# Kernel optimization log

Measured on AMD Instinct MI355X. Metric: run time of the kernel, lower is better.

Reference implementation:

```python
import jax, jax.numpy as jnp
import numpy as np

N_GRAPHS = 32   # number of graphs (equal-size contiguous segments in `batch`)
SEG_LEN = 512   # nodes per graph
NUM_HEADS = 16
LN_EPS = 1e-5


def setup_inputs() -> dict:
    key = jax.random.key(0)
    ks = jax.random.split(key, 4)
    N = N_GRAPHS * SEG_LEN
    D = 1024
    x = jax.random.normal(ks[0], (N, D), dtype=jnp.float32)
    # contiguous equal-size graph segments (what per-graph batching produces)
    batch = jnp.repeat(jnp.arange(N_GRAPHS, dtype=jnp.int64), SEG_LEN)
    s = 1.0 / np.sqrt(D)
    w_in = jax.random.normal(ks[1], (3 * D, D), dtype=jnp.float32) * s
    b_in = jnp.zeros((3 * D,), dtype=jnp.float32)
    w_out = jax.random.normal(ks[2], (D, D), dtype=jnp.float32) * s
    b_out = jnp.zeros((D,), dtype=jnp.float32)
    gamma = jnp.ones((D,), dtype=jnp.float32)
    beta = jnp.zeros((D,), dtype=jnp.float32)
    return {"x": x, "batch": batch, "w_in": w_in, "b_in": b_in,
            "w_out": w_out, "b_out": b_out, "gamma": gamma, "beta": beta}


def _mha_blockdiag(x, w_in, b_in, w_out, b_out):
    # Packed per-graph self-attention: identical math to looping MHA over each
    # graph's node subset, but done in one dense batched attention.
    N, D = x.shape
    G, S, H = N_GRAPHS, SEG_LEN, NUM_HEADS
    dh = D // H
    qkv = x @ w_in.T + b_in                       # (N, 3D)
    qkv = qkv.reshape(G, S, 3, H, dh)
    q, k, v = qkv[:, :, 0], qkv[:, :, 1], qkv[:, :, 2]  # (G, S, H, dh)
    scale = 1.0 / jnp.sqrt(jnp.asarray(dh, x.dtype))
    scores = jnp.einsum('gqhd,gkhd->ghqk', q, k) * scale  # (G, H, S, S)
    probs = jax.nn.softmax(scores, axis=-1)
    ctx = jnp.einsum('ghqk,gkhd->gqhd', probs, v).reshape(N, D)
    return ctx @ w_out.T + b_out


def reference(x, batch, w_in, b_in, w_out, b_out, gamma, beta):
    attn_out = _mha_blockdiag(x, w_in, b_in, w_out, b_out)
    # dropout is identity in eval mode; residual + LayerNorm
    h = x + attn_out
    mu = jnp.mean(h, axis=-1, keepdims=True)
    var = jnp.var(h, axis=-1, keepdims=True)
    return (h - mu) * jax.lax.rsqrt(var + LN_EPS) * gamma + beta
```

## Files before the change

kernel.cpp:

```cpp
#include <hip/hip_runtime.h>
#include <hip/hip_bf16.h>
#include <math.h>

#define N_TOK  16384
#define DMODEL 1024
#define GRAPHS 32
#define SEGLEN 512
#define HEADS  16
#define DH     64
#define D3     3072
#define QK_LD  2048
#define KDIM   1024
#define NT_K   16

typedef __bf16 bf16;
typedef __attribute__((ext_vector_type(4))) __bf16 bf16x4;
typedef __attribute__((ext_vector_type(8))) __bf16 bf16x8;
typedef __attribute__((ext_vector_type(4))) float f32x4;

__device__ __forceinline__ unsigned pack_bf16(float lo, float hi) {
    unsigned short a = __builtin_bit_cast(unsigned short, (bf16)lo);
    unsigned short b = __builtin_bit_cast(unsigned short, (bf16)hi);
    return (unsigned)a | ((unsigned)b << 16);
}

#define N4_X  (N_TOK * DMODEL / 4)
#define N4_WI (D3 * DMODEL / 4)
#define N4_WO (DMODEL * DMODEL / 4)
__global__ __launch_bounds__(256) void cvt_all(const float* __restrict__ x,
                                               const float* __restrict__ w_in,
                                               const float* __restrict__ w_out,
                                               bf16* __restrict__ xb,
                                               bf16* __restrict__ wb,
                                               bf16* __restrict__ wob) {
    int i = blockIdx.x * blockDim.x + threadIdx.x;
    const float* src; bf16* dst; int j;
    if (i < N4_X)                { src = x;     dst = xb;  j = i; }
    else if (i < N4_X + N4_WI)   { src = w_in;  dst = wb;  j = i - N4_X; }
    else                         { src = w_out; dst = wob; j = i - N4_X - N4_WI; }
    float4 v = ((const float4*)src)[j];
    bf16x4 o;
    o[0] = (bf16)v.x; o[1] = (bf16)v.y; o[2] = (bf16)v.z; o[3] = (bf16)v.w;
    ((bf16x4*)dst)[j] = o;
}

template<int EPI, int VSPLIT>
__global__ __launch_bounds__(256, 3) void gemm128(
    const bf16* __restrict__ A, const bf16* __restrict__ B,
    const float* __restrict__ bias, const float* __restrict__ resid,
    void* __restrict__ C, bf16* __restrict__ vT, int N, int nbn, int ldc)
{
    __shared__ bf16x8 smA[1024];
    __shared__ bf16x8 smB[1024];
    const int tid  = threadIdx.x;
    const int lane = tid & 63, w = tid >> 6;
    const int wr = w >> 1, wc = w & 1;
    const int l15 = lane & 15, l4 = lane >> 4;
    const int r7 = l15 & 7;

    const int nwg  = (int)gridDim.x;
    const int x    = (int)blockIdx.x & 7;
    const int c    = (int)blockIdx.x >> 3;
    const int nmtx = (nwg >> 3) / nbn;
    const int gsz  = nmtx * 8;
    const int grp  = c / gsz;
    const int rem  = c - grp * gsz;
    const int mt   = x * nmtx + (rem >> 3);
    const int nt   = grp * 8 + (rem & 7);
    const int bm0  = mt * 128, bn0 = nt * 128;

    const int srow = tid >> 3, skb = tid & 7;

    uint4 pa[4], pb[4];
    auto PF_LOAD = [&](int t) {
        const int k0 = t * 64;
        #pragma unroll
        for (int q = 0; q < 4; q++) {
            int row = q * 32 + srow;
            pa[q] = *(const uint4*)(A + (size_t)(bm0 + row) * KDIM + k0 + skb * 8);
            pb[q] = *(const uint4*)(B + (size_t)(bn0 + row) * KDIM + k0 + skb * 8);
        }
    };
    auto LDS_WRITE = [&]() {
        #pragma unroll
        for (int q = 0; q < 4; q++) {
            int row = q * 32 + srow;
            smA[row * 8 + (skb ^ (row & 7))] = __builtin_bit_cast(bf16x8, pa[q]);
            smB[row * 8 + (skb ^ (row & 7))] = __builtin_bit_cast(bf16x8, pb[q]);
        }
    };

    f32x4 acc[4][4] = {};

    PF_LOAD(0);
    LDS_WRITE();
    __syncthreads();

    #pragma unroll 1
    for (int t = 0; t < NT_K; ++t) {
        if (t + 1 < NT_K) PF_LOAD(t + 1);
        #pragma unroll
        for (int kp = 0; kp < 2; kp++) {
            const int slot = kp * 4 + l4;
            bf16x8 af[4], bfr[4];
            #pragma unroll
            for (int m = 0; m < 4; m++)
                af[m] = smA[(wr * 64 + m * 16 + l15) * 8 + (slot ^ r7)];
            #pragma unroll
            for (int n = 0; n < 4; n++)
                bfr[n] = smB[(wc * 64 + n * 16 + l15) * 8 + (slot ^ r7)];
            #pragma unroll
            for (int m = 0; m < 4; m++)
                #pragma unroll
                for (int n = 0; n < 4; n++)
                    acc[m][n] = __builtin_amdgcn_mfma_f32_16x16x32_bf16(af[m], bfr[n], acc[m][n], 0, 0, 0);
        }
        __syncthreads();
        if (t + 1 < NT_K) {
            LDS_WRITE();
            __syncthreads();
        }
    }

    #pragma unroll
    for (int m = 0; m < 4; m++) {
        #pragma unroll
        for (int n = 0; n < 4; n++) {
            const int col  = bn0 + wc * 64 + n * 16 + l15;
            const int row0 = bm0 + wr * 64 + m * 16 + l4 * 4;
            const float bv = bias[col];
            if (EPI == 1) {
                #pragma unroll
                for (int i = 0; i < 4; i++) {
                    float v = acc[m][n][i] + bv + resid[(size_t)(row0 + i) * N + col];
                    ((bf16*)C)[(size_t)(row0 + i) * ldc + col] = (bf16)v;
                }
            } else if (VSPLIT && bn0 >= 2048) {
                const int cc = col - 2048;
                bf16x4 pk;
                #pragma unroll
                for (int i = 0; i < 4; i++) pk[i] = (bf16)(acc[m][n][i] + bv);
                *(bf16x4*)(vT + ((size_t)((row0 >> 9) * HEADS + (cc >> 6)) * DH + (cc & 63)) * SEGLEN
                               + (row0 & (SEGLEN - 1))) = pk;
            } else {
                const float sc = (VSPLIT && bn0 < 1024) ? 0.125f : 1.0f;
                #pragma unroll
                for (int i = 0; i < 4; i++)
                    ((bf16*)C)[(size_t)(row0 + i) * ldc + col] = (bf16)((acc[m][n][i] + bv) * sc);
            }
        }
    }
}

__global__ __launch_bounds__(256) void attn_kernel(
    const bf16* __restrict__ qkA, const bf16* __restrict__ vT, bf16* __restrict__ ctx)
{
    const int qt = blockIdx.x, h = blockIdx.y, g = blockIdx.z;
    __shared__ bf16x8 smK[2][64 * 8];
    __shared__ bf16x8 smV[2][64 * 8];
    __shared__ bf16 smP[128 * 64];
    const int tid = threadIdx.x, lane = tid & 63, w = tid >> 6;
    const int l15 = lane & 15, l4 = lane >> 4;
    const int r7 = l15 & 7;
    const int grow0 = g * SEGLEN, qbase = qt * 128;
    const size_t vbase = (size_t)(g * HEADS + h) * DH * SEGLEN;

    bf16x8 qf[2][2];
    #pragma unroll
    for (int m = 0; m < 2; m++)
        #pragma unroll
        for (int kp = 0; kp < 2; kp++)
            qf[m][kp] = *(const bf16x8*)(qkA + (size_t)(grow0 + qbase + w * 32 + m * 16 + l15) * QK_LD
                                          + h * 64 + (kp * 4 + l4) * 8);

    f32x4 acc[2][4] = {};
    float mcol[2] = { -INFINITY, -INFINITY };
    float lcol[2] = { 0.f, 0.f };

    uint4 kr[2][2], vr[2][2];
    auto LOADT = [&](int t, int dst) {
        #pragma unroll
        for (int q = 0; q < 2; q++) {
            int c = tid + 256 * q, r = c >> 3, cb = c & 7;
            kr[dst][q] = *(const uint4*)(qkA + (size_t)(grow0 + t * 64 + r) * QK_LD + 1024 + h * 64 + cb * 8);
            vr[dst][q] = *(const uint4*)(vT + vbase + (size_t)r * SEGLEN + t * 64 + cb * 8);
        }
    };
    LOADT(0, 0);

    #pragma unroll
    for (int t = 0; t < 8; t++) {
        const int cur = t & 1;
        #pragma unroll
        for (int q = 0; q < 2; q++) {
            int c = tid + 256 * q, r = c >> 3, cb = c & 7;
            smK[cur][r * 8 + (cb ^ (r & 7))] = __builtin_bit_cast(bf16x8, kr[cur][q]);
            smV[cur][r * 8 + (cb ^ (r & 7))] = __builtin_bit_cast(bf16x8, vr[cur][q]);
        }
        if (t < 7) LOADT(t + 1, cur ^ 1);
        __syncthreads();

        f32x4 st[4][2] = {};
        #pragma unroll
        for (int kp = 0; kp < 2; kp++) {
            #pragma unroll
            for (int n = 0; n < 4; n++) {
                bf16x8 kf = smK[cur][(n * 16 + l15) * 8 + ((kp * 4 + l4) ^ r7)];
                #pragma unroll
                for (int m = 0; m < 2; m++)
                    st[n][m] = __builtin_amdgcn_mfma_f32_16x16x32_bf16(kf, qf[m][kp], st[n][m], 0, 0, 0);
            }
        }
        float mx[2];
        int need = 0;
        #pragma unroll
        for (int m = 0; m < 2; m++) {
            float a = fmaxf(fmaxf(st[0][m][0], st[0][m][1]), fmaxf(st[0][m][2], st[0][m][3]));
            float b = fmaxf(fmaxf(st[1][m][0], st[1][m][1]), fmaxf(st[1][m][2], st[1][m][3]));
            float c = fmaxf(fmaxf(st[2][m][0], st[2][m][1]), fmaxf(st[2][m][2], st[2][m][3]));
            float d = fmaxf(fmaxf(st[3][m][0], st[3][m][1]), fmaxf(st[3][m][2], st[3][m][3]));
            float m0 = fmaxf(fmaxf(a, b), fmaxf(c, d));
            m0 = fmaxf(m0, __shfl_xor(m0, 16));
            m0 = fmaxf(m0, __shfl_xor(m0, 32));
            mx[m] = m0;
            need |= (m0 > mcol[m] + 8.0f) ? 1 : 0;
        }
        if (__any(need)) {
            #pragma unroll
            for (int m = 0; m < 2; m++) {
                float mn = fmaxf(mcol[m], mx[m]);
                float alpha = __expf(mcol[m] - mn);
                mcol[m] = mn;
                lcol[m] *= alpha;
                float a0 = __shfl(alpha, l4 * 4 + 0);
                float a1 = __shfl(alpha, l4 * 4 + 1);
                float a2 = __shfl(alpha, l4 * 4 + 2);
                float a3 = __shfl(alpha, l4 * 4 + 3);
                #pragma unroll
                for (int n = 0; n < 4; n++) {
                    acc[m][n][0] *= a0; acc[m][n][1] *= a1;
                    acc[m][n][2] *= a2; acc[m][n][3] *= a3;
                }
            }
        }
        unsigned* smPd = (unsigned*)smP;
        #pragma unroll
        for (int m = 0; m < 2; m++) {
            const int prow = w * 32 + m * 16 + l15;
            const int pb = prow * 32;
            float rs = 0.f;
            #pragma unroll
            for (int n = 0; n < 4; n++) {
                float p0 = __expf(st[n][m][0] - mcol[m]);
                float p1 = __expf(st[n][m][1] - mcol[m]);
                float p2 = __expf(st[n][m][2] - mcol[m]);
                float p3 = __expf(st[n][m][3] - mcol[m]);
                rs += (p0 + p1) + (p2 + p3);
                const int cb = ((n * 16 + l4 * 4) ^ (r7 << 3)) >> 1;
                smPd[pb + cb]     = pack_bf16(p0, p1);
                smPd[pb + cb + 1] = pack_bf16(p2, p3);
            }
            rs += __shfl_xor(rs, 16);
            rs += __shfl_xor(rs, 32);
            lcol[m] += rs;
        }
        #pragma unroll
        for (int kp = 0; kp < 2; kp++) {
            bf16x8 pf[2];
            #pragma unroll
            for (int m = 0; m < 2; m++)
                pf[m] = ((const bf16x8*)smP)[(w * 32 + m * 16 + l15) * 8 + ((kp * 4 + l4) ^ r7)];
            #pragma unroll
            for (int n = 0; n < 4; n++) {
                bf16x8 vf = smV[cur][(n * 16 + l15) * 8 + ((kp * 4 + l4) ^ r7)];
                #pragma unroll
                for (int m = 0; m < 2; m++)
                    acc[m][n] = __builtin_amdgcn_mfma_f32_16x16x32_bf16(pf[m], vf, acc[m][n], 0, 0, 0);
            }
        }
    }

    #pragma unroll
    for (int m = 0; m < 2; m++) {
        float li0 = 1.f / __shfl(lcol[m], l4 * 4 + 0);
        float li1 = 1.f / __shfl(lcol[m], l4 * 4 + 1);
        float li2 = 1.f / __shfl(lcol[m], l4 * 4 + 2);
        float li3 = 1.f / __shfl(lcol[m], l4 * 4 + 3);
        float linv[4] = { li0, li1, li2, li3 };
        #pragma unroll
        for (int i = 0; i < 4; i++) {
            int row = grow0 + qbase + w * 32 + m * 16 + l4 * 4 + i;
            #pragma unroll
            for (int n = 0; n < 4; n++) {
                int col = h * 64 + n * 16 + l15;
                ctx[(size_t)row * DMODEL + col] = (bf16)(acc[m][n][i] * linv[i]);
            }
        }
    }
}

__global__ __launch_bounds__(256) void ln_kernel(
    const bf16* __restrict__ h, const float* __restrict__ gamma,
    const float* __restrict__ beta, float* __restrict__ out)
{
    const int row = blockIdx.x;
    bf16x4 hv = ((const bf16x4*)(h + (size_t)row * DMODEL))[threadIdx.x];
    float v0 = (float)hv[0], v1 = (float)hv[1], v2 = (float)hv[2], v3 = (float)hv[3];
    float s  = v0 + v1 + v2 + v3;
    float ss = v0 * v0 + v1 * v1 + v2 * v2 + v3 * v3;
    #pragma unroll
    for (int d = 1; d < 64; d <<= 1) { s += __shfl_xor(s, d); ss += __shfl_xor(ss, d); }
    __shared__ float red[8];
    int wv = threadIdx.x >> 6, lane = threadIdx.x & 63;
    if (lane == 0) { red[wv] = s; red[4 + wv] = ss; }
    __syncthreads();
    s  = red[0] + red[1] + red[2] + red[3];
    ss = red[4] + red[5] + red[6] + red[7];
    float mu  = s * (1.f / 1024.f);
    float var = ss * (1.f / 1024.f) - mu * mu;
    float rs  = rsqrtf(var + 1e-5f);
    float4 gv = ((const float4*)gamma)[threadIdx.x];
    float4 bv = ((const float4*)beta)[threadIdx.x];
    float4 o;
    o.x = (v0 - mu) * rs * gv.x + bv.x;
    o.y = (v1 - mu) * rs * gv.y + bv.y;
    o.z = (v2 - mu) * rs * gv.z + bv.z;
    o.w = (v3 - mu) * rs * gv.w + bv.w;
    ((float4*)(out + (size_t)row * DMODEL))[threadIdx.x] = o;
}

extern "C" void kernel_launch(void* const* d_in, const int* in_sizes, int n_in,
                              void* d_out, int out_size, void* d_ws, size_t ws_size,
                              hipStream_t stream) {
    const float* x     = (const float*)d_in[0];
    const float* w_in  = (const float*)d_in[2];
    const float* b_in  = (const float*)d_in[3];
    const float* w_out = (const float*)d_in[4];
    const float* b_out = (const float*)d_in[5];
    const float* gamma = (const float*)d_in[6];
    const float* beta  = (const float*)d_in[7];
    float* out = (float*)d_out;

    char* ws = (char*)d_ws;
    bf16*  xb   = (bf16*)ws;
    bf16*  wb   = (bf16*)(ws + 33554432);
    bf16*  wob  = (bf16*)(ws + 39845888);
    bf16*  qkA  = (bf16*)(ws + 41943040);
    bf16*  vT   = (bf16*)(ws + 109051904);
    bf16*  ctxb = xb;
    bf16*  hbuf = qkA;

    cvt_all<<<(N4_X + N4_WI + N4_WO) / 256, 256, 0, stream>>>(x, w_in, w_out, xb, wb, wob);

    gemm128<0, 1><<<3072, 256, 0, stream>>>(xb, wb, b_in, nullptr, qkA, vT,
                                            D3, 24, QK_LD);
    attn_kernel<<<dim3(4, 16, 32), 256, 0, stream>>>(qkA, vT, ctxb);

    gemm128<1, 0><<<1024, 256, 0, stream>>>(ctxb, wob, b_out, x, hbuf, nullptr,
                                            DMODEL, 8, DMODEL);
    ln_kernel<<<N_TOK, 256, 0, stream>>>(hbuf, gamma, beta, out);
}
```

Measured before the change: 272.6 us.

## Use async global-to-LDS loads in attention, exp2 softmax, bf16 residual

```diff
diff --git a/kernel.cpp b/kernel.cpp
--- a/kernel.cpp
+++ b/kernel.cpp
@@ -18,10 +18,18 @@
 typedef __attribute__((ext_vector_type(8))) __bf16 bf16x8;
 typedef __attribute__((ext_vector_type(4))) float f32x4;
 
+#define QSCALE 0.180336880f
+
 __device__ __forceinline__ unsigned pack_bf16(float lo, float hi) {
     unsigned short a = __builtin_bit_cast(unsigned short, (bf16)lo);
     unsigned short b = __builtin_bit_cast(unsigned short, (bf16)hi);
     return (unsigned)a | ((unsigned)b << 16);
+}
+
+__device__ __forceinline__ void async_copy16(const void* g, void* l) {
+    __builtin_amdgcn_global_load_lds(
+        (const __attribute__((address_space(1))) void*)g,
+        (__attribute__((address_space(3))) void*)l, 16, 0, 0);
 }
 
 #define N4_X  (N_TOK * DMODEL / 4)
@@ -44,10 +52,11 @@
     ((bf16x4*)dst)[j] = o;
 }
 
-template<int EPI, int VSPLIT>
+template<int RES, int VSPLIT>
 __global__ __launch_bounds__(256, 3) void gemm128(
     const bf16* __restrict__ A, const bf16* __restrict__ B,
-    const float* __restrict__ bias, const float* __restrict__ resid,
+    const float* __restrict__ bias, const bf16* __restrict__ residb,
+    const float* __restrict__ residf,
     void* __restrict__ C, bf16* __restrict__ vT, int N, int nbn, int ldc)
 {
     __shared__ bf16x8 smA[1024];
@@ -129,10 +138,16 @@
             const int col  = bn0 + wc * 64 + n * 16 + l15;
             const int row0 = bm0 + wr * 64 + m * 16 + l4 * 4;
             const float bv = bias[col];
-            if (EPI == 1) {
+            if (RES == 1) {
                 #pragma unroll
                 for (int i = 0; i < 4; i++) {
-                    float v = acc[m][n][i] + bv + resid[(size_t)(row0 + i) * N + col];
+                    float v = acc[m][n][i] + bv + (float)residb[(size_t)(row0 + i) * N + col];
+                    ((bf16*)C)[(size_t)(row0 + i) * ldc + col] = (bf16)v;
+                }
+            } else if (RES == 2) {
+                #pragma unroll
+                for (int i = 0; i < 4; i++) {
+                    float v = acc[m][n][i] + bv + residf[(size_t)(row0 + i) * N + col];
                     ((bf16*)C)[(size_t)(row0 + i) * ldc + col] = (bf16)v;
                 }
             } else if (VSPLIT && bn0 >= 2048) {
@@ -143,7 +158,7 @@
                 *(bf16x4*)(vT + ((size_t)((row0 >> 9) * HEADS + (cc >> 6)) * DH + (cc & 63)) * SEGLEN
                                + (row0 & (SEGLEN - 1))) = pk;
             } else {
-                const float sc = (VSPLIT && bn0 < 1024) ? 0.125f : 1.0f;
+                const float sc = (VSPLIT && bn0 < 1024) ? QSCALE : 1.0f;
                 #pragma unroll
                 for (int i = 0; i < 4; i++)
                     ((bf16*)C)[(size_t)(row0 + i) * ldc + col] = (bf16)((acc[m][n][i] + bv) * sc);
@@ -165,6 +180,21 @@
     const int grow0 = g * SEGLEN, qbase = qt * 128;
     const size_t vbase = (size_t)(g * HEADS + h) * DH * SEGLEN;
 
+    auto ISSUE = [&](int t, int dst) {
+        #pragma unroll
+        for (int q = 0; q < 2; q++) {
+            int c = q * 256 + tid;
+            int r = c >> 3, cb = c & 7;
+            int cbs = cb ^ (r & 7);
+            async_copy16(qkA + (size_t)(grow0 + t * 64 + r) * QK_LD + 1024 + h * 64 + cbs * 8,
+                         (char*)&smK[dst][0] + c * 16);
+            async_copy16(vT + vbase + (size_t)r * SEGLEN + t * 64 + cbs * 8,
+                         (char*)&smV[dst][0] + c * 16);
+        }
+    };
+
+    ISSUE(0, 0);
+
     bf16x8 qf[2][2];
     #pragma unroll
     for (int m = 0; m < 2; m++)
@@ -177,28 +207,12 @@
     float mcol[2] = { -INFINITY, -INFINITY };
     float lcol[2] = { 0.f, 0.f };
 
-    uint4 kr[2][2], vr[2][2];
-    auto LOADT = [&](int t, int dst) {
-        #pragma unroll
-        for (int q = 0; q < 2; q++) {
-            int c = tid + 256 * q, r = c >> 3, cb = c & 7;
-            kr[dst][q] = *(const uint4*)(qkA + (size_t)(grow0 + t * 64 + r) * QK_LD + 1024 + h * 64 + cb * 8);
-            vr[dst][q] = *(const uint4*)(vT + vbase + (size_t)r * SEGLEN + t * 64 + cb * 8);
-        }
-    };
-    LOADT(0, 0);
+    __syncthreads();
 
     #pragma unroll
     for (int t = 0; t < 8; t++) {
         const int cur = t & 1;
-        #pragma unroll
-        for (int q = 0; q < 2; q++) {
-            int c = tid + 256 * q, r = c >> 3, cb = c & 7;
-            smK[cur][r * 8 + (cb ^ (r & 7))] = __builtin_bit_cast(bf16x8, kr[cur][q]);
-            smV[cur][r * 8 + (cb ^ (r & 7))] = __builtin_bit_cast(bf16x8, vr[cur][q]);
-        }
-        if (t < 7) LOADT(t + 1, cur ^ 1);
-        __syncthreads();
+        if (t < 7) ISSUE(t + 1, cur ^ 1);
 
         f32x4 st[4][2] = {};
         #pragma unroll
@@ -229,7 +243,7 @@
             #pragma unroll
             for (int m = 0; m < 2; m++) {
                 float mn = fmaxf(mcol[m], mx[m]);
-                float alpha = __expf(mcol[m] - mn);
+                float alpha = exp2f(mcol[m] - mn);
                 mcol[m] = mn;
                 lcol[m] *= alpha;
                 float a0 = __shfl(alpha, l4 * 4 + 0);
@@ -251,10 +265,10 @@
             float rs = 0.f;
             #pragma unroll
             for (int n = 0; n < 4; n++) {
-                float p0 = __expf(st[n][m][0] - mcol[m]);
-                float p1 = __expf(st[n][m][1] - mcol[m]);
-                float p2 = __expf(st[n][m][2] - mcol[m]);
-                float p3 = __expf(st[n][m][3] - mcol[m]);
+                float p0 = exp2f(st[n][m][0] - mcol[m]);
+                float p1 = exp2f(st[n][m][1] - mcol[m]);
+                float p2 = exp2f(st[n][m][2] - mcol[m]);
+                float p3 = exp2f(st[n][m][3] - mcol[m]);
                 rs += (p0 + p1) + (p2 + p3);
                 const int cb = ((n * 16 + l4 * 4) ^ (r7 << 3)) >> 1;
                 smPd[pb + cb]     = pack_bf16(p0, p1);
@@ -278,6 +292,7 @@
                     acc[m][n] = __builtin_amdgcn_mfma_f32_16x16x32_bf16(pf[m], vf, acc[m][n], 0, 0, 0);
             }
         }
+        __syncthreads();
     }
 
     #pragma unroll
@@ -347,16 +362,21 @@
     bf16*  wob  = (bf16*)(ws + 39845888);
     bf16*  qkA  = (bf16*)(ws + 41943040);
     bf16*  vT   = (bf16*)(ws + 109051904);
-    bf16*  ctxb = xb;
     bf16*  hbuf = qkA;
+    const bool ctx_sep = (ws_size >= (size_t)176160768);
+    bf16*  ctxb = ctx_sep ? (bf16*)(ws + 142606336) : xb;
 
     cvt_all<<<(N4_X + N4_WI + N4_WO) / 256, 256, 0, stream>>>(x, w_in, w_out, xb, wb, wob);
 
-    gemm128<0, 1><<<3072, 256, 0, stream>>>(xb, wb, b_in, nullptr, qkA, vT,
+    gemm128<0, 1><<<3072, 256, 0, stream>>>(xb, wb, b_in, nullptr, nullptr, qkA, vT,
                                             D3, 24, QK_LD);
     attn_kernel<<<dim3(4, 16, 32), 256, 0, stream>>>(qkA, vT, ctxb);
 
-    gemm128<1, 0><<<1024, 256, 0, stream>>>(ctxb, wob, b_out, x, hbuf, nullptr,
-                                            DMODEL, 8, DMODEL);
+    if (ctx_sep)
+        gemm128<1, 0><<<1024, 256, 0, stream>>>(ctxb, wob, b_out, xb, nullptr, hbuf, nullptr,
+                                                DMODEL, 8, DMODEL);
+    else
+        gemm128<2, 0><<<1024, 256, 0, stream>>>(ctxb, wob, b_out, nullptr, x, hbuf, nullptr,
+                                                DMODEL, 8, DMODEL);
     ln_kernel<<<N_TOK, 256, 0, stream>>>(hbuf, gamma, beta, out);
 }
```

Result: slower. 292.7 us (+7.4%).
